# Kernel tuning notes

Measured on AMD Instinct MI355X. Metric: run time of the kernel, lower is better.

Reference implementation:

```python
import jax, jax.numpy as jnp
import numpy as np

WINDOW = 5
SIGMA = 4.0
KSIZE = 2 * int(4.0 * SIGMA + 0.5) + 1  # 33, matches torchvision GaussianBlur setup

H1, W1, B, N, C = 56, 56, 16, 32, 512
PAD = WINDOW - 1


def _gauss_kernel():
    x = jnp.arange(KSIZE, dtype=jnp.float32) - (KSIZE - 1) / 2.0
    k = jnp.exp(-0.5 * (x / SIGMA) ** 2)
    return k / jnp.sum(k)


def _blur(img):
    # separable Gaussian blur with reflect padding (torchvision GaussianBlur default)
    k = _gauss_kernel()
    p = KSIZE // 2
    x = jnp.pad(img, ((0, 0), (0, 0), (p, p), (p, p)), mode='reflect')
    dn = ('NCHW', 'OIHW', 'NCHW')
    x = jax.lax.conv_general_dilated(x, k.reshape(1, 1, KSIZE, 1), (1, 1), 'VALID', dimension_numbers=dn)
    x = jax.lax.conv_general_dilated(x, k.reshape(1, 1, 1, KSIZE), (1, 1), 'VALID', dimension_numbers=dn)
    return x


def _forward(embeddings, memory_bank, out_h, out_w):
    H, W, Bb, Cc = embeddings.shape
    x_norm = jnp.sum(embeddings * embeddings, axis=-1, keepdims=True)  # H W B 1
    best = None
    for d1 in range(WINDOW):
        for d2 in range(WINDOW):
            y = memory_bank[d1:H + d1, d2:W + d2]            # H W N C (shifted slice)
            y_norm = jnp.sum(y * y, axis=-1)                  # H W N
            cross = jnp.einsum('hwbc,hwnc->hwbn', embeddings, y)
            dsq = jnp.maximum(x_norm - 2.0 * cross + y_norm[:, :, None, :], 0.0)
            dmin = jnp.sqrt(jnp.min(dsq, axis=-1))            # H W B
            best = dmin if best is None else jnp.minimum(best, dmin)
    pix = jnp.transpose(best, (2, 0, 1))[:, None, :, :]        # B 1 H W
    img = jnp.max(pix, axis=(1, 2, 3))                         # B
    pix = jax.image.resize(pix, (Bb, 1, out_h, out_w), method='linear')  # align_corners=False bilinear
    return img, _blur(pix)


def setup_inputs() -> dict:
    key = jax.random.key(0)
    k1, k2 = jax.random.split(key)
    embeddings = jax.random.normal(k1, (H1, W1, B, C), dtype=jnp.float32)
    memory_bank = jax.random.normal(k2, (H1 + PAD, W1 + PAD, N, C), dtype=jnp.float32)
    return {'embeddings': embeddings, 'memory_bank': memory_bank, 'out_h': 224, 'out_w': 224}


def reference(embeddings, memory_bank, out_h, out_w):
    return _forward(embeddings, memory_bank, out_h, out_w)
```

## Files before the change

### kernel.cpp

```cpp
#include <hip/hip_runtime.h>
#include <math.h>

#define H1 56
#define W1 56
#define BB 16
#define NN 32
#define CC 512
#define MH 60
#define MW 60
#define OH 224
#define OW 224

typedef __bf16 bf16x8 __attribute__((ext_vector_type(8)));
typedef float floatx4 __attribute__((ext_vector_type(4)));

#define MBH_OFF    0
#define F_YN_OFF   29491200
#define F_BEST_OFF 29606400
#define F_TMP1_OFF 29656576
#define F_TOTAL_FLOATS 29857280ull

#define S_XN_OFF   0
#define S_YN_OFF   50176
#define S_BEST_OFF 165376
#define S_TMP1_OFF 215552

#define GLOAD_LDS16(g, l) __builtin_amdgcn_global_load_lds( \
    (const __attribute__((address_space(1))) unsigned int*)(g), \
    (__attribute__((address_space(3))) unsigned int*)(l), 16, 0, 0)

__global__ void cvt_norm_kernel(const float* __restrict__ src, __bf16* __restrict__ dsth,
                                float* __restrict__ norm, int nvec) {
    int wid  = (int)((blockIdx.x * blockDim.x + threadIdx.x) >> 6);
    int lane = threadIdx.x & 63;
    if (wid >= nvec) return;
    const float* p = src + (size_t)wid * CC + lane * 8;
    floatx4 a = *(const floatx4*)p;
    floatx4 b = *(const floatx4*)(p + 4);
    if (dsth) {
        bf16x8 v;
        v[0] = (__bf16)a.x; v[1] = (__bf16)a.y; v[2] = (__bf16)a.z; v[3] = (__bf16)a.w;
        v[4] = (__bf16)b.x; v[5] = (__bf16)b.y; v[6] = (__bf16)b.z; v[7] = (__bf16)b.w;
        *(bf16x8*)(dsth + (size_t)wid * CC + lane * 8) = v;
    }
    float s = a.x*a.x + a.y*a.y + a.z*a.z + a.w*a.w
            + b.x*b.x + b.y*b.y + b.z*b.z + b.w*b.w;
    s += __shfl_xor(s, 32, 64);
    s += __shfl_xor(s, 16, 64);
    s += __shfl_xor(s, 8, 64);
    s += __shfl_xor(s, 4, 64);
    s += __shfl_xor(s, 2, 64);
    s += __shfl_xor(s, 1, 64);
    if (lane == 0) norm[wid] = s;
}

#define BSTRIDE 520
#define HROWS 16
#define NHS (6 * 8 * 2)

__global__ __launch_bounds__(256, 2) void dist_kernel_bf16(
        const float* __restrict__ emb, const __bf16* __restrict__ mbh,
        const float* __restrict__ ynorm, float* __restrict__ best) {
    __shared__ __bf16 Bs[4][HROWS * BSTRIDE];
    __shared__ float Ys[6 * 8 * NN];

    int bx0  = blockIdx.x;
    int bx   = (bx0 & 7) * 49 + (bx0 >> 3);
    int h0   = (bx / 14) * 2;
    int w0   = (bx % 14) * 4;
    int tid  = threadIdx.x;
    int wave = tid >> 6;
    int lane = tid & 63;
    int nrow = lane & 15;
    int seg  = lane >> 4;
    int w    = w0 + wave;

    bf16x8 afragA[16], afragB[16];
    float snA = 0.f, snB = 0.f;
    const float* apA = emb + ((size_t)(h0 * W1 + w) * BB + nrow) * CC + seg * 8;
    const float* apB = apA + (size_t)W1 * BB * CC;
#pragma unroll
    for (int kk = 0; kk < 16; kk++) {
        floatx4 a0 = *(const floatx4*)(apA + kk * 32);
        floatx4 a1 = *(const floatx4*)(apA + kk * 32 + 4);
        floatx4 b0 = *(const floatx4*)(apB + kk * 32);
        floatx4 b1 = *(const floatx4*)(apB + kk * 32 + 4);
        bf16x8 va, vb;
        va[0] = (__bf16)a0.x; va[1] = (__bf16)a0.y; va[2] = (__bf16)a0.z; va[3] = (__bf16)a0.w;
        va[4] = (__bf16)a1.x; va[5] = (__bf16)a1.y; va[6] = (__bf16)a1.z; va[7] = (__bf16)a1.w;
        vb[0] = (__bf16)b0.x; vb[1] = (__bf16)b0.y; vb[2] = (__bf16)b0.z; vb[3] = (__bf16)b0.w;
        vb[4] = (__bf16)b1.x; vb[5] = (__bf16)b1.y; vb[6] = (__bf16)b1.z; vb[7] = (__bf16)b1.w;
        afragA[kk] = va; afragB[kk] = vb;
        snA += a0.x*a0.x + a0.y*a0.y + a0.z*a0.z + a0.w*a0.w
             + a1.x*a1.x + a1.y*a1.y + a1.z*a1.z + a1.w*a1.w;
        snB += b0.x*b0.x + b0.y*b0.y + b0.z*b0.z + b0.w*b0.w
             + b1.x*b1.x + b1.y*b1.y + b1.z*b1.z + b1.w*b1.w;
    }
    snA += __shfl_xor(snA, 16, 64); snA += __shfl_xor(snA, 32, 64);
    snB += __shfl_xor(snB, 16, 64); snB += __shfl_xor(snB, 32, 64);
    floatx4 xnA, xnB;
#pragma unroll
    for (int r = 0; r < 4; r++) {
        xnA[r] = __shfl(snA, seg * 4 + r, 64);
        xnB[r] = __shfl(snB, seg * 4 + r, 64);
    }

    for (int idx = tid; idx < 6 * 8 * NN; idx += 256) {
        int row = idx >> 8;
        int c   = idx & 255;
        Ys[idx] = ynorm[((size_t)((h0 + row) * MW + w0)) * NN + c];
    }

    float bvA[4] = {1e30f, 1e30f, 1e30f, 1e30f};
    float bvB[4] = {1e30f, 1e30f, 1e30f, 1e30f};

#pragma unroll
    for (int t = 0; t < 3; t++) {
        int p  = t >> 1;
        int hh = t & 1;
        const __bf16* bp = mbh + ((size_t)((h0 + (p >> 3)) * MW + (w0 + (p & 7))) * NN
                                  + hh * HROWS) * CC;
#pragma unroll
        for (int tt = 0; tt < 4; tt++) {
            int n = wave * 4 + tt;
            GLOAD_LDS16(bp + (size_t)n * CC + lane * 8, &Bs[t][n * BSTRIDE]);
        }
    }
    asm volatile("s_waitcnt lgkmcnt(0)" ::: "memory");

    int sidx = 0;
    for (int rr = 0; rr < 6; rr++) {
        bool a0 = (rr < 5);
        bool a1 = (rr >= 1);
        for (int j = 0; j < 8; j++) {
            int d2 = j - wave;
            bool act = (d2 >= 0 && d2 < 5);
            const float* yrow = &Ys[(rr * 8 + j) * NN];
#pragma unroll
            for (int hh = 0; hh < 2; hh++, sidx++) {
                int slot = sidx & 3;
                __builtin_amdgcn_sched_barrier(0);
                if (sidx < NHS - 2) {
                    asm volatile("s_waitcnt vmcnt(8)" ::: "memory");
                } else if (sidx == NHS - 2) {
                    asm volatile("s_waitcnt vmcnt(4)" ::: "memory");
                } else {
                    asm volatile("s_waitcnt vmcnt(0)" ::: "memory");
                }
                __builtin_amdgcn_sched_barrier(0);
                __builtin_amdgcn_s_barrier();

                int t3 = sidx + 3;
                if (t3 < NHS) {
                    int p3  = t3 >> 1;
                    int hh3 = t3 & 1;
                    const __bf16* bp = mbh + ((size_t)((h0 + (p3 >> 4)) * MW
                                          + (w0 + ((p3 >> 1) & 7))) * NN + hh3 * HROWS) * CC;
#pragma unroll
                    for (int tt = 0; tt < 4; tt++) {
                        int n = wave * 4 + tt;
                        GLOAD_LDS16(bp + (size_t)n * CC + lane * 8, &Bs[t3 & 3][n * BSTRIDE]);
                    }
                }

                if (act) {
                    const __bf16* Bc = &Bs[slot][0];
                    float yn = yrow[nrow + hh * 16];
                    floatx4 cA = {0,0,0,0}, cB = {0,0,0,0};
#pragma unroll
                    for (int kk = 0; kk < 16; kk++) {
                        bf16x8 b = *(const bf16x8*)(Bc + nrow * BSTRIDE + kk * 32 + seg * 8);
                        cA = __builtin_amdgcn_mfma_f32_16x16x32_bf16(afragA[kk], b, cA, 0, 0, 0);
                        cB = __builtin_amdgcn_mfma_f32_16x16x32_bf16(afragB[kk], b, cB, 0, 0, 0);
                    }
                    if (a0) {
#pragma unroll
                        for (int r = 0; r < 4; r++)
                            bvA[r] = fminf(bvA[r], fmaxf(xnA[r] - 2.f * cA[r] + yn, 0.f));
                    }
                    if (a1) {
#pragma unroll
                        for (int r = 0; r < 4; r++)
                            bvB[r] = fminf(bvB[r], fmaxf(xnB[r] - 2.f * cB[r] + yn, 0.f));
                    }
                }
            }
        }
    }

#pragma unroll
    for (int r = 0; r < 4; r++) {
        float v = bvA[r];
        v = fminf(v, __shfl_xor(v, 1, 64));
        v = fminf(v, __shfl_xor(v, 2, 64));
        v = fminf(v, __shfl_xor(v, 4, 64));
        v = fminf(v, __shfl_xor(v, 8, 64));
        bvA[r] = v;
        float u = bvB[r];
        u = fminf(u, __shfl_xor(u, 1, 64));
        u = fminf(u, __shfl_xor(u, 2, 64));
        u = fminf(u, __shfl_xor(u, 4, 64));
        u = fminf(u, __shfl_xor(u, 8, 64));
        bvB[r] = u;
    }
    if ((lane & 15) == 0) {
        int posA = h0 * W1 + w;
        int posB = (h0 + 1) * W1 + w;
#pragma unroll
        for (int r = 0; r < 4; r++) {
            int b = seg * 4 + r;
            best[(size_t)b * (H1 * W1) + posA] = sqrtf(bvA[r]);
            best[(size_t)b * (H1 * W1) + posB] = sqrtf(bvB[r]);
        }
    }
}

__global__ __launch_bounds__(256) void dist_kernel_f32(
        const float* __restrict__ emb, const float* __restrict__ mb,
        const float* __restrict__ xnorm, const float* __restrict__ ynorm,
        float* __restrict__ best) {
    __shared__ __bf16 Bs[NN * BSTRIDE];
    int bx   = blockIdx.x;
    int h    = bx / 14;
    int w0   = (bx % 14) * 4;
    int tid  = threadIdx.x;
    int wave = tid >> 6;
    int lane = tid & 63;
    int nrow = lane & 15;
    int seg  = lane >> 4;
    int w    = w0 + wave;

    bf16x8 afrag[16];
    const float* ap = emb + ((size_t)(h * W1 + w) * BB + nrow) * CC + seg * 8;
#pragma unroll
    for (int kk = 0; kk < 16; kk++) {
        floatx4 f0 = *(const floatx4*)(ap + kk * 32);
        floatx4 f1 = *(const floatx4*)(ap + kk * 32 + 4);
        bf16x8 v;
        v[0] = (__bf16)f0.x; v[1] = (__bf16)f0.y; v[2] = (__bf16)f0.z; v[3] = (__bf16)f0.w;
        v[4] = (__bf16)f1.x; v[5] = (__bf16)f1.y; v[6] = (__bf16)f1.z; v[7] = (__bf16)f1.w;
        afrag[kk] = v;
    }
    floatx4 xn = *(const floatx4*)(xnorm + (size_t)(h * W1 + w) * BB + seg * 4);
    float bestv[4] = {1e30f, 1e30f, 1e30f, 1e30f};

    for (int d1 = 0; d1 < 5; d1++) {
        int mr = h + d1;
        for (int j = 0; j < 8; j++) {
            int mc = w0 + j;
            const float* bp = mb + (size_t)(mr * MW + mc) * NN * CC;
            __syncthreads();
#pragma unroll
            for (int t = 0; t < 8; t++) {
                int c0 = t * 256 + tid;
                int n  = c0 >> 6;
                int ks = (c0 & 63) << 3;
                floatx4 f0 = *(const floatx4*)(bp + n * CC + ks);
                floatx4 f1 = *(const floatx4*)(bp + n * CC + ks + 4);
                bf16x8 v;
                v[0] = (__bf16)f0.x; v[1] = (__bf16)f0.y; v[2] = (__bf16)f0.z; v[3] = (__bf16)f0.w;
                v[4] = (__bf16)f1.x; v[5] = (__bf16)f1.y; v[6] = (__bf16)f1.z; v[7] = (__bf16)f1.w;
                *(bf16x8*)(&Bs[n * BSTRIDE + ks]) = v;
            }
            __syncthreads();

            int d2 = j - wave;
            if (d2 >= 0 && d2 < 5) {
                float yn0 = ynorm[(size_t)(mr * MW + mc) * NN + nrow];
                float yn1 = ynorm[(size_t)(mr * MW + mc) * NN + nrow + 16];
                floatx4 acc0 = {0,0,0,0};
                floatx4 acc1 = {0,0,0,0};
#pragma unroll
                for (int kk = 0; kk < 16; kk++) {
                    bf16x8 b0 = *(const bf16x8*)(&Bs[nrow * BSTRIDE + kk * 32 + seg * 8]);
                    bf16x8 b1 = *(const bf16x8*)(&Bs[(nrow + 16) * BSTRIDE + kk * 32 + seg * 8]);
                    acc0 = __builtin_amdgcn_mfma_f32_16x16x32_bf16(afrag[kk], b0, acc0, 0, 0, 0);
                    acc1 = __builtin_amdgcn_mfma_f32_16x16x32_bf16(afrag[kk], b1, acc1, 0, 0, 0);
                }
#pragma unroll
                for (int r = 0; r < 4; r++) {
                    float d0  = fmaxf(xn[r] - 2.f * acc0[r] + yn0, 0.f);
                    float d1v = fmaxf(xn[r] - 2.f * acc1[r] + yn1, 0.f);
                    bestv[r] = fminf(bestv[r], fminf(d0, d1v));
                }
            }
        }
    }
#pragma unroll
    for (int r = 0; r < 4; r++) {
        float v = bestv[r];
        v = fminf(v, __shfl_xor(v, 1, 64));
        v = fminf(v, __shfl_xor(v, 2, 64));
        v = fminf(v, __shfl_xor(v, 4, 64));
        v = fminf(v, __shfl_xor(v, 8, 64));
        bestv[r] = v;
    }
    if ((lane & 15) == 0) {
        int pos = h * W1 + w;
#pragma unroll
        for (int r = 0; r < 4; r++) {
            int b = seg * 4 + r;
            best[(size_t)b * (H1 * W1) + pos] = sqrtf(bestv[r]);
        }
    }
}

__global__ void max_kernel(const float* __restrict__ best, float* __restrict__ out) {
    __shared__ float red[256];
    int b = blockIdx.x;
    float m = 0.f;
    for (int i = threadIdx.x; i < H1 * W1; i += 256)
        m = fmaxf(m, best[(size_t)b * (H1 * W1) + i]);
    red[threadIdx.x] = m;
    __syncthreads();
    for (int s = 128; s > 0; s >>= 1) {
        if (threadIdx.x < s) red[threadIdx.x] = fmaxf(red[threadIdx.x], red[threadIdx.x + s]);
        __syncthreads();
    }
    if (threadIdx.x == 0) out[b] = red[0];
}

struct GaussK { float k[33]; };

__device__ __forceinline__ int refl(int i, int n) {
    i = (i < 0) ? -i : i;
    i = (i > n - 1) ? 2 * (n - 1) - i : i;
    return i;
}

__global__ void vblur_kernel(const float* __restrict__ best, float* __restrict__ tmp1, GaussK g) {
    int idx = blockIdx.x * 256 + threadIdx.x;
    int lx = idx % W1;
    int y  = (idx / W1) % OH;
    int b  = idx / (W1 * OH);
    const float* p = best + (size_t)b * (H1 * W1);
    float acc = 0.f;
#pragma unroll
    for (int u = 0; u < 33; u++) {
        int z  = refl(y - 16 + u, OH);
        int rz = z & 3;
        float t = 0.125f + 0.25f * (float)((rz + 2) & 3);
        int lo = (z >> 2) + ((rz < 2) ? -1 : 0);
        int hi = min(lo + 1, H1 - 1);
        lo = max(lo, 0);
        acc += g.k[u] * ((1.f - t) * p[lo * W1 + lx] + t * p[hi * W1 + lx]);
    }
    tmp1[idx] = acc;
}

__global__ void hblur_kernel(const float* __restrict__ tmp1, float* __restrict__ dst, GaussK g) {
    int idx = blockIdx.x * 256 + threadIdx.x;
    int x = idx % OW;
    int y = (idx / OW) % OH;
    int b = idx / (OW * OH);
    const float* p = tmp1 + ((size_t)b * OH + y) * W1;
    float acc = 0.f;
#pragma unroll
    for (int u = 0; u < 33; u++) {
        int z  = refl(x - 16 + u, OW);
        int rz = z & 3;
        float t = 0.125f + 0.25f * (float)((rz + 2) & 3);
        int lo = (z >> 2) + ((rz < 2) ? -1 : 0);
        int hi = min(lo + 1, W1 - 1);
        lo = max(lo, 0);
        acc += g.k[u] * ((1.f - t) * p[lo] + t * p[hi]);
    }
    dst[idx] = acc;
}

extern "C" void kernel_launch(void* const* d_in, const int* in_sizes, int n_in,
                              void* d_out, int out_size, void* d_ws, size_t ws_size,
                              hipStream_t stream) {
    const float* emb = (const float*)d_in[0];
    const float* mbp = (const float*)d_in[1];
    float* ws  = (float*)d_ws;
    float* out = (float*)d_out;

    bool big = ws_size >= F_TOTAL_FLOATS * 4ull;

    float* best;
    float* tmp1;

    if (big) {
        __bf16* mbh  = (__bf16*)(ws + MBH_OFF);
        float* ynorm = ws + F_YN_OFF;
        best = ws + F_BEST_OFF;
        tmp1 = ws + F_TMP1_OFF;
        cvt_norm_kernel<<<(MH * MW * NN) / 4, 256, 0, stream>>>(mbp, mbh, ynorm, MH * MW * NN);
        dist_kernel_bf16<<<28 * 14, 256, 0, stream>>>(emb, mbh, ynorm, best);
    } else {
        float* xnorm = ws + S_XN_OFF;
        float* ynorm = ws + S_YN_OFF;
        best = ws + S_BEST_OFF;
        tmp1 = ws + S_TMP1_OFF;
        cvt_norm_kernel<<<(H1 * W1 * BB) / 4, 256, 0, stream>>>(emb, nullptr, xnorm, H1 * W1 * BB);
        cvt_norm_kernel<<<(MH * MW * NN) / 4, 256, 0, stream>>>(mbp, nullptr, ynorm, MH * MW * NN);
        dist_kernel_f32<<<H1 * 14, 256, 0, stream>>>(emb, mbp, xnorm, ynorm, best);
    }

    max_kernel<<<BB, 256, 0, stream>>>(best, out);

    GaussK g;
    {
        double wsum = 0.0, wd[33];
        for (int u = 0; u < 33; u++) {
            double xk = (u - 16) / 4.0;
            wd[u] = exp(-0.5 * xk * xk);
            wsum += wd[u];
        }
        for (int u = 0; u < 33; u++) g.k[u] = (float)(wd[u] / wsum);
    }
    vblur_kernel<<<(BB * OH * W1) / 256, 256, 0, stream>>>(best, tmp1, g);
    hblur_kernel<<<(BB * OH * OW) / 256, 256, 0, stream>>>(tmp1, out + 16, g);
}
```

Measured before the change: 534.8 us.

## Load memory-bank fragments directly into registers instead of shared LDS pipeline

Removes the shared-memory staging of memory-bank tiles (global_load_lds ring buffer with barriers) and the LDS copy of y-norms. Each wave now loads its own B fragments straight from global memory into registers with a two-set double buffer and reads y-norms directly. This drops the block-wide barriers and the inactive-wave iterations, but it gives up the reuse of tiles shared across the four waves, which raises global/L2 traffic and register pressure.

```diff
diff --git a/kernel.cpp b/kernel.cpp
--- a/kernel.cpp
+++ b/kernel.cpp
@@ -24,10 +24,6 @@
 #define S_YN_OFF   50176
 #define S_BEST_OFF 165376
 #define S_TMP1_OFF 215552
-
-#define GLOAD_LDS16(g, l) __builtin_amdgcn_global_load_lds( \
-    (const __attribute__((address_space(1))) unsigned int*)(g), \
-    (__attribute__((address_space(3))) unsigned int*)(l), 16, 0, 0)
 
 __global__ void cvt_norm_kernel(const float* __restrict__ src, __bf16* __restrict__ dsth,
                                 float* __restrict__ norm, int nvec) {
@@ -54,16 +50,9 @@
     if (lane == 0) norm[wid] = s;
 }
 
-#define BSTRIDE 520
-#define HROWS 16
-#define NHS (6 * 8 * 2)
-
 __global__ __launch_bounds__(256, 2) void dist_kernel_bf16(
         const float* __restrict__ emb, const __bf16* __restrict__ mbh,
         const float* __restrict__ ynorm, float* __restrict__ best) {
-    __shared__ __bf16 Bs[4][HROWS * BSTRIDE];
-    __shared__ float Ys[6 * 8 * NN];
-
     int bx0  = blockIdx.x;
     int bx   = (bx0 & 7) * 49 + (bx0 >> 3);
     int h0   = (bx / 14) * 2;
@@ -105,88 +94,58 @@
         xnB[r] = __shfl(snB, seg * 4 + r, 64);
     }
 
-    for (int idx = tid; idx < 6 * 8 * NN; idx += 256) {
-        int row = idx >> 8;
-        int c   = idx & 255;
-        Ys[idx] = ynorm[((size_t)((h0 + row) * MW + w0)) * NN + c];
-    }
-
     float bvA[4] = {1e30f, 1e30f, 1e30f, 1e30f};
     float bvB[4] = {1e30f, 1e30f, 1e30f, 1e30f};
 
-#pragma unroll
-    for (int t = 0; t < 3; t++) {
-        int p  = t >> 1;
-        int hh = t & 1;
-        const __bf16* bp = mbh + ((size_t)((h0 + (p >> 3)) * MW + (w0 + (p & 7))) * NN
-                                  + hh * HROWS) * CC;
-#pragma unroll
-        for (int tt = 0; tt < 4; tt++) {
-            int n = wave * 4 + tt;
-            GLOAD_LDS16(bp + (size_t)n * CC + lane * 8, &Bs[t][n * BSTRIDE]);
-        }
-    }
-    asm volatile("s_waitcnt lgkmcnt(0)" ::: "memory");
-
-    int sidx = 0;
-    for (int rr = 0; rr < 6; rr++) {
-        bool a0 = (rr < 5);
-        bool a1 = (rr >= 1);
-        for (int j = 0; j < 8; j++) {
-            int d2 = j - wave;
-            bool act = (d2 >= 0 && d2 < 5);
-            const float* yrow = &Ys[(rr * 8 + j) * NN];
-#pragma unroll
-            for (int hh = 0; hh < 2; hh++, sidx++) {
-                int slot = sidx & 3;
-                __builtin_amdgcn_sched_barrier(0);
-                if (sidx < NHS - 2) {
-                    asm volatile("s_waitcnt vmcnt(8)" ::: "memory");
-                } else if (sidx == NHS - 2) {
-                    asm volatile("s_waitcnt vmcnt(4)" ::: "memory");
-                } else {
-                    asm volatile("s_waitcnt vmcnt(0)" ::: "memory");
-                }
-                __builtin_amdgcn_sched_barrier(0);
-                __builtin_amdgcn_s_barrier();
-
-                int t3 = sidx + 3;
-                if (t3 < NHS) {
-                    int p3  = t3 >> 1;
-                    int hh3 = t3 & 1;
-                    const __bf16* bp = mbh + ((size_t)((h0 + (p3 >> 4)) * MW
-                                          + (w0 + ((p3 >> 1) & 7))) * NN + hh3 * HROWS) * CC;
-#pragma unroll
-                    for (int tt = 0; tt < 4; tt++) {
-                        int n = wave * 4 + tt;
-                        GLOAD_LDS16(bp + (size_t)n * CC + lane * 8, &Bs[t3 & 3][n * BSTRIDE]);
-                    }
-                }
-
-                if (act) {
-                    const __bf16* Bc = &Bs[slot][0];
-                    float yn = yrow[nrow + hh * 16];
-                    floatx4 cA = {0,0,0,0}, cB = {0,0,0,0};
-#pragma unroll
-                    for (int kk = 0; kk < 16; kk++) {
-                        bf16x8 b = *(const bf16x8*)(Bc + nrow * BSTRIDE + kk * 32 + seg * 8);
-                        cA = __builtin_amdgcn_mfma_f32_16x16x32_bf16(afragA[kk], b, cA, 0, 0, 0);
-                        cB = __builtin_amdgcn_mfma_f32_16x16x32_bf16(afragB[kk], b, cB, 0, 0, 0);
-                    }
-                    if (a0) {
-#pragma unroll
-                        for (int r = 0; r < 4; r++)
-                            bvA[r] = fminf(bvA[r], fmaxf(xnA[r] - 2.f * cA[r] + yn, 0.f));
-                    }
-                    if (a1) {
-#pragma unroll
-                        for (int r = 0; r < 4; r++)
-                            bvB[r] = fminf(bvB[r], fmaxf(xnB[r] - 2.f * cB[r] + yn, 0.f));
-                    }
-                }
-            }
-        }
-    }
+    const __bf16* laneoff = mbh + (size_t)nrow * CC + seg * 8;
+
+    int rr_l = 0, d2_l = 0, hh_l = 0, q_l = 0;
+
+#define QPTR() (laneoff + ((size_t)((h0 + rr_l) * MW + (w + d2_l)) * NN + hh_l * 16) * CC + q_l * 256)
+#define ADVQ() { q_l ^= 1; if (!q_l) { hh_l ^= 1; if (!hh_l) { d2_l++; if (d2_l == 5) { d2_l = 0; rr_l++; } } } }
+#define LOADSET(S) { const __bf16* _p = QPTR(); \
+    S[0] = *(const bf16x8*)(_p);        S[1] = *(const bf16x8*)(_p + 32); \
+    S[2] = *(const bf16x8*)(_p + 64);   S[3] = *(const bf16x8*)(_p + 96); \
+    S[4] = *(const bf16x8*)(_p + 128);  S[5] = *(const bf16x8*)(_p + 160); \
+    S[6] = *(const bf16x8*)(_p + 192);  S[7] = *(const bf16x8*)(_p + 224); \
+    ADVQ(); }
+
+    bf16x8 S0[8], S1[8];
+    LOADSET(S0);
+
+    int rr_c = 0, d2_c = 0, hh_c = 0;
+    floatx4 cA, cB;
+
+    for (int i = 0; i < 60; i++) {
+        LOADSET(S1);
+        float yn = ynorm[(size_t)((h0 + rr_c) * MW + (w + d2_c)) * NN + hh_c * 16 + nrow];
+
+        cA = floatx4{0,0,0,0}; cB = floatx4{0,0,0,0};
+#pragma unroll
+        for (int k = 0; k < 8; k++) {
+            cA = __builtin_amdgcn_mfma_f32_16x16x32_bf16(afragA[k], S0[k], cA, 0, 0, 0);
+            cB = __builtin_amdgcn_mfma_f32_16x16x32_bf16(afragB[k], S0[k], cB, 0, 0, 0);
+        }
+        if (i < 59) LOADSET(S0);
+#pragma unroll
+        for (int k = 0; k < 8; k++) {
+            cA = __builtin_amdgcn_mfma_f32_16x16x32_bf16(afragA[8 + k], S1[k], cA, 0, 0, 0);
+            cB = __builtin_amdgcn_mfma_f32_16x16x32_bf16(afragB[8 + k], S1[k], cB, 0, 0, 0);
+        }
+
+        bool va = (rr_c < 5), vb = (rr_c >= 1);
+#pragma unroll
+        for (int r = 0; r < 4; r++) {
+            float dA = fmaxf(xnA[r] - 2.f * cA[r] + yn, 0.f);
+            float dB = fmaxf(xnB[r] - 2.f * cB[r] + yn, 0.f);
+            bvA[r] = fminf(bvA[r], va ? dA : 1e30f);
+            bvB[r] = fminf(bvB[r], vb ? dB : 1e30f);
+        }
+        hh_c ^= 1; if (!hh_c) { d2_c++; if (d2_c == 5) { d2_c = 0; rr_c++; } }
+    }
+#undef QPTR
+#undef ADVQ
+#undef LOADSET
 
 #pragma unroll
     for (int r = 0; r < 4; r++) {
@@ -214,6 +173,8 @@
         }
     }
 }
+
+#define BSTRIDE 520
 
 __global__ __launch_bounds__(256) void dist_kernel_f32(
         const float* __restrict__ emb, const float* __restrict__ mb,
```

New measurement: 632.3 us. +18.2%, slower.
